# Kernel tuning notes

Measured on AMD Instinct MI355X. Metric: run time of the kernel, lower is better.

## Reference

```python
import jax, jax.numpy as jnp
import numpy as np

NPOINT = 1024
RADIUS = 0.2
NSAMPLE = 64
BN_EPS = 1e-5


def setup_inputs() -> dict:
    key = jax.random.key(0)
    ks = jax.random.split(key, 16)
    B, N = 8, 8192
    inp = {
        "xyz": jax.random.normal(ks[0], (B, 3, N), jnp.float32),
        "points": jax.random.normal(ks[1], (B, 3, N), jnp.float32),
        "seed_inds": jax.random.randint(ks[2], (B, N), 0, N),
    }
    chans = [6, 64, 64, 128]
    for i in range(3):
        cin, cout = chans[i], chans[i + 1]
        kk = jax.random.split(ks[3 + i], 3)
        inp[f"w{i}"] = jax.random.normal(kk[0], (cout, cin), jnp.float32) / np.sqrt(cin)
        inp[f"b{i}"] = jnp.zeros((cout,), jnp.float32)
        inp[f"g{i}"] = jnp.ones((cout,), jnp.float32)
        inp[f"be{i}"] = jnp.zeros((cout,), jnp.float32)
        inp[f"m{i}"] = jax.random.normal(kk[1], (cout,), jnp.float32) * 0.1
        inp[f"v{i}"] = jax.random.uniform(kk[2], (cout,), jnp.float32, 0.5, 1.5)
    return inp


def _fps(xyz, npoint):
    # xyz: [B, N, 3]. Deterministic start at index 0 (torch uses a random start).
    B, N, _ = xyz.shape

    def step(carry, _):
        dist, far = carry
        cent = jnp.take_along_axis(xyz, far[:, None, None], axis=1)  # [B,1,3]
        d = jnp.sum((xyz - cent) ** 2, -1)                           # [B,N]
        dist = jnp.minimum(dist, d)
        nxt = jnp.argmax(dist, -1)
        return (dist, nxt), far

    init = (jnp.full((B, N), 1e10, xyz.dtype), jnp.zeros((B,), jnp.int32))
    _, idxs = jax.lax.scan(step, init, None, length=npoint)
    return idxs.T  # [B, npoint]


def _sqdist(src, dst):
    # src [B,S,3], dst [B,N,3] -> [B,S,N]
    d = -2.0 * jnp.einsum("bsc,bnc->bsn", src, dst)
    d += jnp.sum(src ** 2, -1)[:, :, None]
    d += jnp.sum(dst ** 2, -1)[:, None, :]
    return d


def _gather(pts, idx):
    # pts [B,N,C], idx [B,S,K] -> [B,S,K,C]
    B, S, K = idx.shape
    flat = jnp.take_along_axis(pts, idx.reshape(B, S * K, 1), axis=1)
    return flat.reshape(B, S, K, pts.shape[-1])


def _forward(xyz, points, seed_inds, layers):
    xyz_t = xyz.transpose(0, 2, 1)      # [B,N,3]
    pts_t = points.transpose(0, 2, 1)   # [B,N,D]
    B, N, _ = xyz_t.shape

    fps_idx = _fps(xyz_t, NPOINT)                                   # [B,S]
    new_seed = jnp.take_along_axis(seed_inds, fps_idx.astype(seed_inds.dtype), axis=1)
    new_xyz = jnp.take_along_axis(xyz_t, fps_idx[:, :, None], axis=1)  # [B,S,3]

    # ball query via sort trick (same math as torch module)
    sq = _sqdist(new_xyz, xyz_t)                                    # [B,S,N]
    gi = jnp.where(sq > RADIUS ** 2, N, jnp.arange(N, dtype=jnp.int32)[None, None, :])
    gi = jnp.sort(gi, axis=-1)[:, :, :NSAMPLE]                      # [B,S,K]
    first = gi[:, :, :1]
    gi = jnp.where(gi == N, first, gi)

    gxyz = _gather(xyz_t, gi) - new_xyz[:, :, None, :]              # [B,S,K,3]
    gpts = _gather(pts_t, gi)                                       # [B,S,K,D]
    feat = jnp.concatenate([gxyz, gpts], -1)                        # [B,S,K,3+D]

    for (w, b, g, be, m, v) in layers:
        feat = jnp.einsum("bskc,oc->bsko", feat, w) + b             # 1x1 conv
        feat = (feat - m) * (g / jnp.sqrt(v + BN_EPS)) + be         # BN (inference)
        feat = jax.nn.relu(feat)

    new_points = jnp.max(feat, axis=2).transpose(0, 2, 1)           # [B,Cout,S]
    return new_xyz.transpose(0, 2, 1), new_points, new_seed


def reference(xyz, points, seed_inds,
              w0, b0, g0, be0, m0, v0,
              w1, b1, g1, be1, m1, v1,
              w2, b2, g2, be2, m2, v2):
    layers = [(w0, b0, g0, be0, m0, v0),
              (w1, b1, g1, be1, m1, v1),
              (w2, b2, g2, be2, m2, v2)]
    return _forward(xyz, points, seed_inds, layers)
```

## Files before the change

### kernel.cpp

```cpp
#include <hip/hip_runtime.h>

#define B_ 8
#define N_ 8192
#define S_ 1024
#define NS_ 64

typedef float v2f __attribute__((ext_vector_type(2)));
typedef unsigned long long u64;
typedef short bf16x8 __attribute__((ext_vector_type(8)));
typedef float f32x4 __attribute__((ext_vector_type(4)));

#define OUT0 0
#define OUT1 24576
#define OUT2 1073152

template <int CTRL>
static __device__ __forceinline__ float dpp_max_step(float v) {
    int o = __builtin_amdgcn_update_dpp(__float_as_int(v), __float_as_int(v),
                                        CTRL, 0xf, 0xf, false);
    return fmaxf(v, __int_as_float(o));
}
static __device__ __forceinline__ float wave_max_f32(float v) {
    v = dpp_max_step<0x111>(v);
    v = dpp_max_step<0x112>(v);
    v = dpp_max_step<0x114>(v);
    v = dpp_max_step<0x118>(v);
    v = dpp_max_step<0x142>(v);
    v = dpp_max_step<0x143>(v);
    return __int_as_float(__builtin_amdgcn_readlane(__float_as_int(v), 63));
}
template <int CTRL>
static __device__ __forceinline__ unsigned dpp_umin_step(unsigned v) {
    unsigned o = (unsigned)__builtin_amdgcn_update_dpp((int)v, (int)v,
                                                       CTRL, 0xf, 0xf, false);
    return v < o ? v : o;
}
static __device__ __forceinline__ unsigned wave_min_u32(unsigned v) {
    v = dpp_umin_step<0x111>(v);
    v = dpp_umin_step<0x112>(v);
    v = dpp_umin_step<0x114>(v);
    v = dpp_umin_step<0x118>(v);
    v = dpp_umin_step<0x142>(v);
    v = dpp_umin_step<0x143>(v);
    return (unsigned)__builtin_amdgcn_readlane((int)v, 63);
}

static __device__ __forceinline__ short f2bf(float f) {
    unsigned u = __float_as_uint(f);
    return (short)((u + 0x7FFFu + ((u >> 16) & 1u)) >> 16);
}

#define FPS_T 256
#define FPS_J 16

__global__ __launch_bounds__(FPS_T, 1) void fps_kernel(const float* __restrict__ xyz,
                                                       float* out) {
    const int b = blockIdx.x;
    const int t = threadIdx.x;
    const int lane = t & 63;
    const int wq = t >> 6;
    const float* X = xyz + b * 3 * N_;

    __shared__ float4 xyzq[N_];
    __shared__ u64 slots[8];
    __shared__ float seedL[S_];

    v2f px2[FPS_J], py2[FPS_J], pz2[FPS_J], dist2[FPS_J];
#pragma unroll
    for (int j = 0; j < FPS_J; ++j) {
        int n = t + 512 * j;
        float x0 = X[n],          x1 = X[n + 256];
        float y0 = X[N_ + n],     y1 = X[N_ + n + 256];
        float z0 = X[2 * N_ + n], z1 = X[2 * N_ + n + 256];
        px2[j] = (v2f){x0, x1};
        py2[j] = (v2f){y0, y1};
        pz2[j] = (v2f){z0, z1};
        dist2[j] = (v2f){1e10f, 1e10f};
        xyzq[n]       = make_float4(x0, y0, z0, 0.f);
        xyzq[n + 256] = make_float4(x1, y1, z1, 0.f);
    }
    __syncthreads();

    int ci = 0;
    float c0 = X[0], c1 = X[N_], c2 = X[2 * N_];

    for (int step = 0; step < S_; ++step) {
        if (t == 0) seedL[step] = __int_as_float(ci);

        v2f mv = (v2f){-1.0f, -1.0f};
        {
#pragma clang fp contract(off)
            v2f c0v = (v2f){c0, c0};
            v2f c1v = (v2f){c1, c1};
            v2f c2v = (v2f){c2, c2};
#pragma unroll
            for (int j = 0; j < FPS_J; ++j) {
                v2f e0 = px2[j] - c0v;
                v2f e1 = py2[j] - c1v;
                v2f e2 = pz2[j] - c2v;
                v2f q0 = e0 * e0;
                v2f q1 = e1 * e1;
                v2f q2 = e2 * e2;
                v2f d  = (q0 + q1) + q2;
                v2f dm = __builtin_elementwise_min(dist2[j], d);
                dist2[j] = dm;
                mv = __builtin_elementwise_max(mv, dm);
            }
        }
        float m = fmaxf(mv.x, mv.y);

        unsigned mask = 0u;
#pragma unroll
        for (int j = 0; j < FPS_J; ++j) {
            if (dist2[j].x == m) mask |= (1u << (2 * j));
            if (dist2[j].y == m) mask |= (1u << (2 * j + 1));
        }
        float wmax = wave_max_f32(m);

        unsigned c = (unsigned)(__ffs(mask) - 1);
        unsigned cand = (m == wmax) ? ((unsigned)t | (c << 8)) : 0xffffffffu;
        unsigned widx = wave_min_u32(cand);

        if (lane == 63) {
            u64 key = ((u64)__float_as_uint(wmax) << 13) | (u64)(8191u - widx);
            slots[((step & 1) << 2) + wq] = key;
        }
        __syncthreads();

        const u64* sp = &slots[(step & 1) << 2];
        u64 k0 = sp[0], k1 = sp[1], k2 = sp[2], k3 = sp[3];
        int i0 = 8191 - (int)(k0 & 0x1fffull);
        int i1 = 8191 - (int)(k1 & 0x1fffull);
        int i2 = 8191 - (int)(k2 & 0x1fffull);
        int i3 = 8191 - (int)(k3 & 0x1fffull);
        float4 p0 = xyzq[i0];
        float4 p1 = xyzq[i1];
        float4 p2 = xyzq[i2];
        float4 p3 = xyzq[i3];
        bool b01 = k0 > k1, b23 = k2 > k3;
        u64 ka = b01 ? k0 : k1;
        u64 kb = b23 ? k2 : k3;
        float4 pa, pb;
        pa.x = b01 ? p0.x : p1.x; pa.y = b01 ? p0.y : p1.y; pa.z = b01 ? p0.z : p1.z;
        pb.x = b23 ? p2.x : p3.x; pb.y = b23 ? p2.y : p3.y; pb.z = b23 ? p2.z : p3.z;
        bool bab = ka > kb;
        u64 km = bab ? ka : kb;
        ci = 8191 - (int)(km & 0x1fffull);
        c0 = bab ? pa.x : pb.x;
        c1 = bab ? pa.y : pb.y;
        c2 = bab ? pa.z : pb.z;
    }

    __syncthreads();
    float* oseed = out + OUT2 + b * S_;
#pragma unroll
    for (int k = 0; k < 4; ++k)
        oseed[t + 256 * k] = seedL[t + 256 * k];
}

__global__ __launch_bounds__(256) void wconv_kernel(const float* __restrict__ w1,
                                                    const float* __restrict__ w2,
                                                    short* __restrict__ wbf) {
    int t = blockIdx.x * 256 + threadIdx.x;
    float v = (t < 4096) ? w1[t] : w2[t - 4096];
    wbf[t] = f2bf(v);
}

__global__ __launch_bounds__(256) void down_kernel(
    const float* __restrict__ xyz, const float* __restrict__ pts,
    const int* __restrict__ seed,
    const float* __restrict__ w0, const float* __restrict__ b0,
    const float* __restrict__ g0, const float* __restrict__ be0,
    const float* __restrict__ m0, const float* __restrict__ v0,
    const float* __restrict__ w1, const float* __restrict__ b1,
    const float* __restrict__ g1, const float* __restrict__ be1,
    const float* __restrict__ m1, const float* __restrict__ v1,
    const float* __restrict__ w2, const float* __restrict__ b2,
    const float* __restrict__ g2, const float* __restrict__ be2,
    const float* __restrict__ m2, const float* __restrict__ v2,
    float* out, const short* __restrict__ wbf) {
    const int sg = blockIdx.x;
    const int b = sg >> 10, s = sg & 1023;
    const int t = threadIdx.x;
    const int lane = t & 63;
    const int wq = __builtin_amdgcn_readfirstlane(t >> 6);
    const int ln = lane & 15;
    const int quad = (lane >> 4) & 3;

    __shared__ float f0[64 * 9];
    __shared__ short featA[64 * 72];
    __shared__ short featB[64 * 72];
    __shared__ float wmaxs[4 * 132];
    __shared__ float scs[256], ofs[256];
    __shared__ int cand[4 * 64];
    __shared__ int cnts[4];
    __shared__ int gis[64];

    const float* X = xyz + b * 3 * N_;

    int ci = __float_as_int(out[OUT2 + sg]) & 8191;
    float cx = X[ci], cy = X[N_ + ci], cz = X[2 * N_ + ci];

    {
        float sc, of;
        if (t < 64) {
            int c = t;
            sc = g0[c] / sqrtf(v0[c] + 1e-5f);
            of = (b0[c] - m0[c]) * sc + be0[c];
        } else if (t < 128) {
            int c = t - 64;
            sc = g1[c] / sqrtf(v1[c] + 1e-5f);
            of = (b1[c] - m1[c]) * sc + be1[c];
        } else {
            int c = t - 128;
            sc = g2[c] / sqrtf(v2[c] + 1e-5f);
            of = (b2[c] - m2[c]) * sc + be2[c];
        }
        scs[t] = sc;
        ofs[t] = of;
    }
    __syncthreads();

    if (t == 0) {
        out[OUT0 + (b * 3 + 0) * S_ + s] = cx;
        out[OUT0 + (b * 3 + 1) * S_ + s] = cy;
        out[OUT0 + (b * 3 + 2) * S_ + s] = cz;
        out[OUT2 + sg] = (float)seed[b * N_ + ci];
    }

    {
        int cnt = 0;
        const int wbase = wq << 11;
#pragma unroll 2
        for (int base = 0; base < 2048; base += 128) {
            int n0 = wbase + base + lane;
            int n1 = n0 + 64;
            float x0 = X[n0], y0 = X[N_ + n0], z0 = X[2 * N_ + n0];
            float x1 = X[n1], y1 = X[N_ + n1], z1 = X[2 * N_ + n1];
            float e0 = x0 - cx, e1 = y0 - cy, e2 = z0 - cz;
            float d0 = fmaf(e2, e2, fmaf(e1, e1, e0 * e0));
            float q0 = x1 - cx, q1 = y1 - cy, q2 = z1 - cz;
            float d1 = fmaf(q2, q2, fmaf(q1, q1, q0 * q0));

            u64 mask0 = __ballot(d0 <= 0.04f);
            if (mask0) {
                int pos = cnt + (int)__popcll(mask0 & ((1ull << lane) - 1ull));
                if ((d0 <= 0.04f) && pos < NS_) cand[(wq << 6) + pos] = n0;
                cnt += (int)__popcll(mask0);
            }
            u64 mask1 = __ballot(d1 <= 0.04f);
            if (mask1) {
                int pos = cnt + (int)__popcll(mask1 & ((1ull << lane) - 1ull));
                if ((d1 <= 0.04f) && pos < NS_) cand[(wq << 6) + pos] = n1;
                cnt += (int)__popcll(mask1);
            }
        }
        if (lane == 0) cnts[wq] = cnt;
    }
    __syncthreads();

    if (t < 64) {
        int k = t;
        int start = 0, sel = -1, firstv = -1;
#pragma unroll
        for (int w = 0; w < 4; ++w) {
            int cw = min(cnts[w], NS_);
            if (firstv < 0 && cw > 0) firstv = cand[(w << 6)];
            if (sel < 0 && k < start + cw) sel = cand[(w << 6) + (k - start)];
            start += cw;
        }
        if (sel < 0) sel = firstv;
        gis[t] = sel;
    }
    __syncthreads();

    if (t < 64) {
        int gidx = gis[t] & 8191;
        const float* P = pts + b * 3 * N_;
        f0[t * 9 + 0] = X[gidx] - cx;
        f0[t * 9 + 1] = X[N_ + gidx] - cy;
        f0[t * 9 + 2] = X[2 * N_ + gidx] - cz;
        f0[t * 9 + 3] = P[gidx];
        f0[t * 9 + 4] = P[N_ + gidx];
        f0[t * 9 + 5] = P[2 * N_ + gidx];
    }
    __syncthreads();

    {
        float in[6];
#pragma unroll
        for (int c = 0; c < 6; ++c) in[c] = f0[lane * 9 + c];
#pragma unroll 1
        for (int i = 0; i < 16; i += 4) {
            int o = wq * 16 + i;
            float a0 = 0.f, a1 = 0.f, a2 = 0.f, a3 = 0.f;
#pragma unroll
            for (int c = 0; c < 6; ++c) {
                float rc = in[c];
                a0 = fmaf(rc, w0[(o + 0) * 6 + c], a0);
                a1 = fmaf(rc, w0[(o + 1) * 6 + c], a1);
                a2 = fmaf(rc, w0[(o + 2) * 6 + c], a2);
                a3 = fmaf(rc, w0[(o + 3) * 6 + c], a3);
            }
            featA[lane * 72 + o + 0] = f2bf(fmaxf(fmaf(a0, scs[o + 0], ofs[o + 0]), 0.f));
            featA[lane * 72 + o + 1] = f2bf(fmaxf(fmaf(a1, scs[o + 1], ofs[o + 1]), 0.f));
            featA[lane * 72 + o + 2] = f2bf(fmaxf(fmaf(a2, scs[o + 2], ofs[o + 2]), 0.f));
            featA[lane * 72 + o + 3] = f2bf(fmaxf(fmaf(a3, scs[o + 3], ofs[o + 3]), 0.f));
        }
    }
    __syncthreads();

    const int arow = 16 * wq + ln;
    const bool usebf = (wbf != nullptr);

    {
        bf16x8 a1f[2];
#pragma unroll
        for (int ks = 0; ks < 2; ++ks)
            a1f[ks] = *(const bf16x8*)&featA[arow * 72 + ks * 32 + quad * 8];

#pragma unroll
        for (int nt = 0; nt < 4; ++nt) {
            f32x4 acc = {0.f, 0.f, 0.f, 0.f};
#pragma unroll
            for (int ks = 0; ks < 2; ++ks) {
                int off = (nt * 16 + ln) * 64 + ks * 32 + quad * 8;
                bf16x8 bf;
                if (usebf) {
                    bf = *(const bf16x8*)&wbf[off];
                } else {
                    const float* wr = w1 + off;
                    float4 p = *(const float4*)wr;
                    float4 q = *(const float4*)(wr + 4);
                    bf = (bf16x8){f2bf(p.x), f2bf(p.y), f2bf(p.z), f2bf(p.w),
                                  f2bf(q.x), f2bf(q.y), f2bf(q.z), f2bf(q.w)};
                }
                acc = __builtin_amdgcn_mfma_f32_16x16x32_bf16(a1f[ks], bf, acc, 0, 0, 0);
            }
            int o = nt * 16 + ln;
            float sc = scs[64 + o], of = ofs[64 + o];
#pragma unroll
            for (int reg = 0; reg < 4; ++reg) {
                float y = fmaxf(fmaf(acc[reg], sc, of), 0.f);
                featB[(16 * wq + quad * 4 + reg) * 72 + o] = f2bf(y);
            }
        }
    }

    {
        bf16x8 a2f[2];
#pragma unroll
        for (int ks = 0; ks < 2; ++ks)
            a2f[ks] = *(const bf16x8*)&featB[arow * 72 + ks * 32 + quad * 8];

#pragma unroll
        for (int nt = 0; nt < 8; ++nt) {
            f32x4 acc = {0.f, 0.f, 0.f, 0.f};
#pragma unroll
            for (int ks = 0; ks < 2; ++ks) {
                int off = (nt * 16 + ln) * 64 + ks * 32 + quad * 8;
                bf16x8 bf;
                if (usebf) {
                    bf = *(const bf16x8*)&wbf[4096 + off];
                } else {
                    const float* wr = w2 + off;
                    float4 p = *(const float4*)wr;
                    float4 q = *(const float4*)(wr + 4);
                    bf = (bf16x8){f2bf(p.x), f2bf(p.y), f2bf(p.z), f2bf(p.w),
                                  f2bf(q.x), f2bf(q.y), f2bf(q.z), f2bf(q.w)};
                }
                acc = __builtin_amdgcn_mfma_f32_16x16x32_bf16(a2f[ks], bf, acc, 0, 0, 0);
            }
            int o = nt * 16 + ln;
            float sc = scs[128 + o], of = ofs[128 + o];
            float m = -1.f;
#pragma unroll
            for (int reg = 0; reg < 4; ++reg) {
                float y = fmaxf(fmaf(acc[reg], sc, of), 0.f);
                m = fmaxf(m, y);
            }
            m = fmaxf(m, __shfl_xor(m, 16, 64));
            m = fmaxf(m, __shfl_xor(m, 32, 64));
            if (lane < 16) wmaxs[wq * 132 + o] = m;
        }
    }
    __syncthreads();

    if (t < 128) {
        float m = fmaxf(fmaxf(wmaxs[0 * 132 + t], wmaxs[1 * 132 + t]),
                        fmaxf(wmaxs[2 * 132 + t], wmaxs[3 * 132 + t]));
        out[OUT1 + (b * 128 + t) * S_ + s] = m;
    }
}

extern "C" void kernel_launch(void* const* d_in, const int* in_sizes, int n_in,
                              void* d_out, int out_size, void* d_ws, size_t ws_size,
                              hipStream_t stream) {
    const float* xyz  = (const float*)d_in[0];
    const float* pts  = (const float*)d_in[1];
    const int*   seed = (const int*)d_in[2];
    const float* w0 = (const float*)d_in[3];
    const float* b0 = (const float*)d_in[4];
    const float* g0 = (const float*)d_in[5];
    const float* be0 = (const float*)d_in[6];
    const float* m0 = (const float*)d_in[7];
    const float* v0 = (const float*)d_in[8];
    const float* w1 = (const float*)d_in[9];
    const float* b1 = (const float*)d_in[10];
    const float* g1 = (const float*)d_in[11];
    const float* be1 = (const float*)d_in[12];
    const float* m1 = (const float*)d_in[13];
    const float* v1 = (const float*)d_in[14];
    const float* w2 = (const float*)d_in[15];
    const float* b2 = (const float*)d_in[16];
    const float* g2 = (const float*)d_in[17];
    const float* be2 = (const float*)d_in[18];
    const float* m2 = (const float*)d_in[19];
    const float* v2 = (const float*)d_in[20];
    float* out = (float*)d_out;

    short* wbf = nullptr;
    if (ws_size >= 12288 * sizeof(short)) {
        wbf = (short*)d_ws;
        wconv_kernel<<<dim3(48), dim3(256), 0, stream>>>(w1, w2, wbf);
    }

    fps_kernel<<<dim3(B_), dim3(FPS_T), 0, stream>>>(xyz, out);
    down_kernel<<<dim3(B_ * S_), dim3(256), 0, stream>>>(xyz, pts, seed,
        w0, b0, g0, be0, m0, v0,
        w1, b1, g1, be1, m1, v1,
        w2, b2, g2, be2, m2, v2,
        out, wbf);
}
```

Measured before the change: 1.208 ms.

## Process two centroids per block to share point scans and weight loads

Each down_kernel block now handles two sampled centroids instead of one, and the grid is halved. The ball-query scan loads each xyz point once and tests it against both centroids. The MLP layers load each weight fragment once and issue MFMAs for both feature tiles. The aim is to halve global xyz and weight traffic and the per-block setup, such as the BN scale/offset computation, at the cost of more shared memory, more registers and fewer blocks in flight.

Result: faster. 1.168 ms, median of 2 (-3.3%).

```diff
diff --git a/kernel.cpp b/kernel.cpp
--- a/kernel.cpp
+++ b/kernel.cpp
@@ -180,26 +180,28 @@
     const float* __restrict__ m2, const float* __restrict__ v2,
     float* out, const short* __restrict__ wbf) {
     const int sg = blockIdx.x;
-    const int b = sg >> 10, s = sg & 1023;
+    const int b = sg >> 9, sp = sg & 511;
+    const int s0 = sp << 1;
     const int t = threadIdx.x;
     const int lane = t & 63;
     const int wq = __builtin_amdgcn_readfirstlane(t >> 6);
     const int ln = lane & 15;
     const int quad = (lane >> 4) & 3;
 
-    __shared__ float f0[64 * 9];
-    __shared__ short featA[64 * 72];
-    __shared__ short featB[64 * 72];
-    __shared__ float wmaxs[4 * 132];
+    __shared__ float f0[2][64 * 9];
+    __shared__ short feat[2][64 * 72];
+    __shared__ float wmaxs[2][4 * 132];
     __shared__ float scs[256], ofs[256];
-    __shared__ int cand[4 * 64];
-    __shared__ int cnts[4];
-    __shared__ int gis[64];
+    __shared__ int cand[2][4 * 64];
+    __shared__ int cnts[2][4];
+    __shared__ int gis[2][64];
 
     const float* X = xyz + b * 3 * N_;
 
-    int ci = __float_as_int(out[OUT2 + sg]) & 8191;
-    float cx = X[ci], cy = X[N_ + ci], cz = X[2 * N_ + ci];
+    int ci0 = __float_as_int(out[OUT2 + b * S_ + s0]) & 8191;
+    int ci1 = __float_as_int(out[OUT2 + b * S_ + s0 + 1]) & 8191;
+    float cx0 = X[ci0], cy0 = X[N_ + ci0], cz0 = X[2 * N_ + ci0];
+    float cx1 = X[ci1], cy1 = X[N_ + ci1], cz1 = X[2 * N_ + ci1];
 
     {
         float sc, of;
@@ -221,15 +223,17 @@
     }
     __syncthreads();
 
-    if (t == 0) {
-        out[OUT0 + (b * 3 + 0) * S_ + s] = cx;
-        out[OUT0 + (b * 3 + 1) * S_ + s] = cy;
-        out[OUT0 + (b * 3 + 2) * S_ + s] = cz;
-        out[OUT2 + sg] = (float)seed[b * N_ + ci];
+    if (t < 2) {
+        int cc = t;
+        int ci = cc ? ci1 : ci0;
+        out[OUT0 + (b * 3 + 0) * S_ + s0 + cc] = cc ? cx1 : cx0;
+        out[OUT0 + (b * 3 + 1) * S_ + s0 + cc] = cc ? cy1 : cy0;
+        out[OUT0 + (b * 3 + 2) * S_ + s0 + cc] = cc ? cz1 : cz0;
+        out[OUT2 + b * S_ + s0 + cc] = (float)seed[b * N_ + ci];
     }
 
     {
-        int cnt = 0;
+        int cnt0 = 0, cnt1 = 0;
         const int wbase = wq << 11;
 #pragma unroll 2
         for (int base = 0; base < 2048; base += 128) {
@@ -237,59 +241,81 @@
             int n1 = n0 + 64;
             float x0 = X[n0], y0 = X[N_ + n0], z0 = X[2 * N_ + n0];
             float x1 = X[n1], y1 = X[N_ + n1], z1 = X[2 * N_ + n1];
-            float e0 = x0 - cx, e1 = y0 - cy, e2 = z0 - cz;
-            float d0 = fmaf(e2, e2, fmaf(e1, e1, e0 * e0));
-            float q0 = x1 - cx, q1 = y1 - cy, q2 = z1 - cz;
-            float d1 = fmaf(q2, q2, fmaf(q1, q1, q0 * q0));
-
-            u64 mask0 = __ballot(d0 <= 0.04f);
-            if (mask0) {
-                int pos = cnt + (int)__popcll(mask0 & ((1ull << lane) - 1ull));
-                if ((d0 <= 0.04f) && pos < NS_) cand[(wq << 6) + pos] = n0;
-                cnt += (int)__popcll(mask0);
-            }
-            u64 mask1 = __ballot(d1 <= 0.04f);
-            if (mask1) {
-                int pos = cnt + (int)__popcll(mask1 & ((1ull << lane) - 1ull));
-                if ((d1 <= 0.04f) && pos < NS_) cand[(wq << 6) + pos] = n1;
-                cnt += (int)__popcll(mask1);
-            }
-        }
-        if (lane == 0) cnts[wq] = cnt;
-    }
-    __syncthreads();
-
-    if (t < 64) {
-        int k = t;
+
+            float e0 = x0 - cx0, e1 = y0 - cy0, e2 = z0 - cz0;
+            float dA0 = fmaf(e2, e2, fmaf(e1, e1, e0 * e0));
+            float f0_ = x0 - cx1, f1_ = y0 - cy1, f2_ = z0 - cz1;
+            float dB0 = fmaf(f2_, f2_, fmaf(f1_, f1_, f0_ * f0_));
+            float q0 = x1 - cx0, q1 = y1 - cy0, q2 = z1 - cz0;
+            float dA1 = fmaf(q2, q2, fmaf(q1, q1, q0 * q0));
+            float r0 = x1 - cx1, r1 = y1 - cy1, r2 = z1 - cz1;
+            float dB1 = fmaf(r2, r2, fmaf(r1, r1, r0 * r0));
+
+            u64 mA0 = __ballot(dA0 <= 0.04f);
+            if (mA0) {
+                int pos = cnt0 + (int)__popcll(mA0 & ((1ull << lane) - 1ull));
+                if ((dA0 <= 0.04f) && pos < NS_) cand[0][(wq << 6) + pos] = n0;
+                cnt0 += (int)__popcll(mA0);
+            }
+            u64 mB0 = __ballot(dB0 <= 0.04f);
+            if (mB0) {
+                int pos = cnt1 + (int)__popcll(mB0 & ((1ull << lane) - 1ull));
+                if ((dB0 <= 0.04f) && pos < NS_) cand[1][(wq << 6) + pos] = n0;
+                cnt1 += (int)__popcll(mB0);
+            }
+            u64 mA1 = __ballot(dA1 <= 0.04f);
+            if (mA1) {
+                int pos = cnt0 + (int)__popcll(mA1 & ((1ull << lane) - 1ull));
+                if ((dA1 <= 0.04f) && pos < NS_) cand[0][(wq << 6) + pos] = n1;
+                cnt0 += (int)__popcll(mA1);
+            }
+            u64 mB1 = __ballot(dB1 <= 0.04f);
+            if (mB1) {
+                int pos = cnt1 + (int)__popcll(mB1 & ((1ull << lane) - 1ull));
+                if ((dB1 <= 0.04f) && pos < NS_) cand[1][(wq << 6) + pos] = n1;
+                cnt1 += (int)__popcll(mB1);
+            }
+        }
+        if (lane == 0) { cnts[0][wq] = cnt0; cnts[1][wq] = cnt1; }
+    }
+    __syncthreads();
+
+    if (t < 128) {
+        int cc = t >> 6, k = t & 63;
         int start = 0, sel = -1, firstv = -1;
 #pragma unroll
         for (int w = 0; w < 4; ++w) {
-            int cw = min(cnts[w], NS_);
-            if (firstv < 0 && cw > 0) firstv = cand[(w << 6)];
-            if (sel < 0 && k < start + cw) sel = cand[(w << 6) + (k - start)];
+            int cw = min(cnts[cc][w], NS_);
+            if (firstv < 0 && cw > 0) firstv = cand[cc][(w << 6)];
+            if (sel < 0 && k < start + cw) sel = cand[cc][(w << 6) + (k - start)];
             start += cw;
         }
         if (sel < 0) sel = firstv;
-        gis[t] = sel;
-    }
-    __syncthreads();
-
-    if (t < 64) {
-        int gidx = gis[t] & 8191;
+        gis[cc][k] = sel;
+    }
+    __syncthreads();
+
+    if (t < 128) {
+        int cc = t >> 6, k = t & 63;
+        int gidx = gis[cc][k] & 8191;
         const float* P = pts + b * 3 * N_;
-        f0[t * 9 + 0] = X[gidx] - cx;
-        f0[t * 9 + 1] = X[N_ + gidx] - cy;
-        f0[t * 9 + 2] = X[2 * N_ + gidx] - cz;
-        f0[t * 9 + 3] = P[gidx];
-        f0[t * 9 + 4] = P[N_ + gidx];
-        f0[t * 9 + 5] = P[2 * N_ + gidx];
-    }
-    __syncthreads();
-
-    {
+        float ccx = cc ? cx1 : cx0;
+        float ccy = cc ? cy1 : cy0;
+        float ccz = cc ? cz1 : cz0;
+        f0[cc][k * 9 + 0] = X[gidx] - ccx;
+        f0[cc][k * 9 + 1] = X[N_ + gidx] - ccy;
+        f0[cc][k * 9 + 2] = X[2 * N_ + gidx] - ccz;
+        f0[cc][k * 9 + 3] = P[gidx];
+        f0[cc][k * 9 + 4] = P[N_ + gidx];
+        f0[cc][k * 9 + 5] = P[2 * N_ + gidx];
+    }
+    __syncthreads();
+
+#pragma unroll 1
+    for (int cc = 0; cc < 2; ++cc) {
         float in[6];
 #pragma unroll
-        for (int c = 0; c < 6; ++c) in[c] = f0[lane * 9 + c];
+        for (int c = 0; c < 6; ++c) in[c] = f0[cc][lane * 9 + c];
 #pragma unroll 1
         for (int i = 0; i < 16; i += 4) {
             int o = wq * 16 + i;
@@ -302,10 +328,10 @@
                 a2 = fmaf(rc, w0[(o + 2) * 6 + c], a2);
                 a3 = fmaf(rc, w0[(o + 3) * 6 + c], a3);
             }
-            featA[lane * 72 + o + 0] = f2bf(fmaxf(fmaf(a0, scs[o + 0], ofs[o + 0]), 0.f));
-            featA[lane * 72 + o + 1] = f2bf(fmaxf(fmaf(a1, scs[o + 1], ofs[o + 1]), 0.f));
-            featA[lane * 72 + o + 2] = f2bf(fmaxf(fmaf(a2, scs[o + 2], ofs[o + 2]), 0.f));
-            featA[lane * 72 + o + 3] = f2bf(fmaxf(fmaf(a3, scs[o + 3], ofs[o + 3]), 0.f));
+            feat[cc][lane * 72 + o + 0] = f2bf(fmaxf(fmaf(a0, scs[o + 0], ofs[o + 0]), 0.f));
+            feat[cc][lane * 72 + o + 1] = f2bf(fmaxf(fmaf(a1, scs[o + 1], ofs[o + 1]), 0.f));
+            feat[cc][lane * 72 + o + 2] = f2bf(fmaxf(fmaf(a2, scs[o + 2], ofs[o + 2]), 0.f));
+            feat[cc][lane * 72 + o + 3] = f2bf(fmaxf(fmaf(a3, scs[o + 3], ofs[o + 3]), 0.f));
         }
     }
     __syncthreads();
@@ -314,14 +340,17 @@
     const bool usebf = (wbf != nullptr);
 
     {
-        bf16x8 a1f[2];
-#pragma unroll
-        for (int ks = 0; ks < 2; ++ks)
-            a1f[ks] = *(const bf16x8*)&featA[arow * 72 + ks * 32 + quad * 8];
+        bf16x8 a1f[2][2];
+#pragma unroll
+        for (int cc = 0; cc < 2; ++cc)
+#pragma unroll
+            for (int ks = 0; ks < 2; ++ks)
+                a1f[cc][ks] = *(const bf16x8*)&feat[cc][arow * 72 + ks * 32 + quad * 8];
 
 #pragma unroll
         for (int nt = 0; nt < 4; ++nt) {
-            f32x4 acc = {0.f, 0.f, 0.f, 0.f};
+            f32x4 acc0 = {0.f, 0.f, 0.f, 0.f};
+            f32x4 acc1 = {0.f, 0.f, 0.f, 0.f};
 #pragma unroll
             for (int ks = 0; ks < 2; ++ks) {
                 int off = (nt * 16 + ln) * 64 + ks * 32 + quad * 8;
@@ -335,27 +364,33 @@
                     bf = (bf16x8){f2bf(p.x), f2bf(p.y), f2bf(p.z), f2bf(p.w),
                                   f2bf(q.x), f2bf(q.y), f2bf(q.z), f2bf(q.w)};
                 }
-                acc = __builtin_amdgcn_mfma_f32_16x16x32_bf16(a1f[ks], bf, acc, 0, 0, 0);
+                acc0 = __builtin_amdgcn_mfma_f32_16x16x32_bf16(a1f[0][ks], bf, acc0, 0, 0, 0);
+                acc1 = __builtin_amdgcn_mfma_f32_16x16x32_bf16(a1f[1][ks], bf, acc1, 0, 0, 0);
             }
             int o = nt * 16 + ln;
             float sc = scs[64 + o], of = ofs[64 + o];
 #pragma unroll
             for (int reg = 0; reg < 4; ++reg) {
-                float y = fmaxf(fmaf(acc[reg], sc, of), 0.f);
-                featB[(16 * wq + quad * 4 + reg) * 72 + o] = f2bf(y);
+                float y0 = fmaxf(fmaf(acc0[reg], sc, of), 0.f);
+                float y1 = fmaxf(fmaf(acc1[reg], sc, of), 0.f);
+                feat[0][(16 * wq + quad * 4 + reg) * 72 + o] = f2bf(y0);
+                feat[1][(16 * wq + quad * 4 + reg) * 72 + o] = f2bf(y1);
             }
         }
     }
 
     {
-        bf16x8 a2f[2];
-#pragma unroll
-        for (int ks = 0; ks < 2; ++ks)
-            a2f[ks] = *(const bf16x8*)&featB[arow * 72 + ks * 32 + quad * 8];
+        bf16x8 a2f[2][2];
+#pragma unroll
+        for (int cc = 0; cc < 2; ++cc)
+#pragma unroll
+            for (int ks = 0; ks < 2; ++ks)
+                a2f[cc][ks] = *(const bf16x8*)&feat[cc][arow * 72 + ks * 32 + quad * 8];
 
 #pragma unroll
         for (int nt = 0; nt < 8; ++nt) {
-            f32x4 acc = {0.f, 0.f, 0.f, 0.f};
+            f32x4 acc0 = {0.f, 0.f, 0.f, 0.f};
+            f32x4 acc1 = {0.f, 0.f, 0.f, 0.f};
 #pragma unroll
             for (int ks = 0; ks < 2; ++ks) {
                 int off = (nt * 16 + ln) * 64 + ks * 32 + quad * 8;
@@ -369,27 +404,34 @@
                     bf = (bf16x8){f2bf(p.x), f2bf(p.y), f2bf(p.z), f2bf(p.w),
                                   f2bf(q.x), f2bf(q.y), f2bf(q.z), f2bf(q.w)};
                 }
-                acc = __builtin_amdgcn_mfma_f32_16x16x32_bf16(a2f[ks], bf, acc, 0, 0, 0);
+                acc0 = __builtin_amdgcn_mfma_f32_16x16x32_bf16(a2f[0][ks], bf, acc0, 0, 0, 0);
+                acc1 = __builtin_amdgcn_mfma_f32_16x16x32_bf16(a2f[1][ks], bf, acc1, 0, 0, 0);
             }
             int o = nt * 16 + ln;
             float sc = scs[128 + o], of = ofs[128 + o];
-            float m = -1.f;
+            float m0_ = -1.f, m1_ = -1.f;
 #pragma unroll
             for (int reg = 0; reg < 4; ++reg) {
-                float y = fmaxf(fmaf(acc[reg], sc, of), 0.f);
-                m = fmaxf(m, y);
-            }
-            m = fmaxf(m, __shfl_xor(m, 16, 64));
-            m = fmaxf(m, __shfl_xor(m, 32, 64));
-            if (lane < 16) wmaxs[wq * 132 + o] = m;
-        }
-    }
-    __syncthreads();
-
-    if (t < 128) {
-        float m = fmaxf(fmaxf(wmaxs[0 * 132 + t], wmaxs[1 * 132 + t]),
-                        fmaxf(wmaxs[2 * 132 + t], wmaxs[3 * 132 + t]));
-        out[OUT1 + (b * 128 + t) * S_ + s] = m;
+                m0_ = fmaxf(m0_, fmaxf(fmaf(acc0[reg], sc, of), 0.f));
+                m1_ = fmaxf(m1_, fmaxf(fmaf(acc1[reg], sc, of), 0.f));
+            }
+            m0_ = fmaxf(m0_, __shfl_xor(m0_, 16, 64));
+            m0_ = fmaxf(m0_, __shfl_xor(m0_, 32, 64));
+            m1_ = fmaxf(m1_, __shfl_xor(m1_, 16, 64));
+            m1_ = fmaxf(m1_, __shfl_xor(m1_, 32, 64));
+            if (lane < 16) {
+                wmaxs[0][wq * 132 + o] = m0_;
+                wmaxs[1][wq * 132 + o] = m1_;
+            }
+        }
+    }
+    __syncthreads();
+
+    {
+        int cc = t >> 7, ch = t & 127;
+        float m = fmaxf(fmaxf(wmaxs[cc][0 * 132 + ch], wmaxs[cc][1 * 132 + ch]),
+                        fmaxf(wmaxs[cc][2 * 132 + ch], wmaxs[cc][3 * 132 + ch]));
+        out[OUT1 + (b * 128 + ch) * S_ + s0 + cc] = m;
     }
 }
 
@@ -426,7 +468,7 @@
     }
 
     fps_kernel<<<dim3(B_), dim3(FPS_T), 0, stream>>>(xyz, out);
-    down_kernel<<<dim3(B_ * S_), dim3(256), 0, stream>>>(xyz, pts, seed,
+    down_kernel<<<dim3(B_ * S_ / 2), dim3(256), 0, stream>>>(xyz, pts, seed,
         w0, b0, g0, be0, m0, v0,
         w1, b1, g1, be1, m1, v1,
         w2, b2, g2, be2, m2, v2,
```
